# Kernel tuning notes

Measured on AMD Instinct MI355X. Metric: run time of the kernel, lower is better.

Reference implementation:

```python
import jax, jax.numpy as jnp
import numpy as np

IN_SIZE = 1024
HID = 2048
OUT = 1024
M_STEPS = 100   # max extra ponder steps -> up to M_STEPS+1 total steps
EPS = 0.01


def setup_inputs() -> dict:
    key = jax.random.key(0)
    ks = jax.random.split(key, 11)
    inv = 1.0 / np.sqrt(HID)

    def unif(k, shape, scale):
        return jax.random.uniform(k, shape, jnp.float32, -scale, scale)

    return {
        "x": jax.random.normal(ks[0], (IN_SIZE,), jnp.float32),
        "h0": jax.random.normal(ks[1], (HID,), jnp.float32) * 0.1,
        "c0": jax.random.normal(ks[2], (HID,), jnp.float32) * 0.1,
        "W_ih": unif(ks[3], (4 * HID, 1 + IN_SIZE), inv),
        "b_ih": unif(ks[4], (4 * HID,), inv),
        "W_hh": unif(ks[5], (4 * HID, HID), inv),
        "b_hh": unif(ks[6], (4 * HID,), inv),
        "w_halt": unif(ks[7], (HID,), inv),
        "b_halt": jnp.ones((1,), jnp.float32),  # fc_halt.bias = 1.0 per source
        "W_out": unif(ks[8], (OUT, HID), inv),
        "b_out": unif(ks[9], (OUT,), inv),
    }


def reference(x, h0, c0, W_ih, b_ih, W_hh, b_hh, w_halt, b_halt, W_out, b_out):
    # Input contribution is constant across steps except the prepended halt flag
    # (1 on first step, 0 after). Precompute it once.
    ih_x = W_ih[:, 1:] @ x + b_ih + b_hh      # (4H,)
    w_flag = W_ih[:, 0]                        # (4H,)

    def step(carry, flag):
        h, c = carry
        gates = ih_x + flag * w_flag + W_hh @ h  # (4H,)
        i, f, g, o = jnp.split(gates, 4)
        i = jax.nn.sigmoid(i)
        f = jax.nn.sigmoid(f)
        g = jnp.tanh(g)
        o = jax.nn.sigmoid(o)
        c = f * c + i * g
        h = o * jnp.tanh(c)
        return (h, c), (h, c)

    flags = jnp.concatenate(
        [jnp.ones((1,), x.dtype), jnp.zeros((M_STEPS,), x.dtype)])
    _, (H, C) = jax.lax.scan(step, (h0, c0), flags)  # (M+1, HID) each

    p = jax.nn.sigmoid(H @ w_halt + b_halt[0])       # (M+1,) halting probs
    csum = jnp.cumsum(p)
    halted = csum >= 1.0 - EPS
    # n = first step where cumulative halt prob crosses threshold, capped at M
    n = jnp.where(jnp.any(halted), jnp.argmax(halted), M_STEPS)
    # remainder r = 1 - sum(p[:n]); csum[n] - p[n] == sum(p[:n])
    r = 1.0 - jnp.where(n > 0, csum[n] - p[n], 0.0)

    idx = jnp.arange(M_STEPS + 1)
    w = jnp.where(idx < n, p, jnp.where(idx == n, r, 0.0))  # (M+1,)

    outputs = H @ W_out.T + b_out                    # (M+1, OUT)
    output = w @ outputs                             # (OUT,) weights sum to 1
    h_out = w @ H                                    # (HID,)
    c_out = w @ C                                    # (HID,)
    ponder = n.astype(x.dtype) + 1.0 + r
    return output, (h_out, c_out), ponder
```

## Files before the change

### kernel.cpp

```cpp
#include <hip/hip_runtime.h>


#define HID    2048
#define INS    1024
#define OUTS   1024
#define MSTEPS 100
#define NBLK   256
#define NTHR   1024
#define NWAVE  16
#define JPB    8
#define RPB    32

__device__ __forceinline__ float wave_reduce(float v) {
    #pragma unroll
    for (int off = 32; off > 0; off >>= 1)
        v += __shfl_down(v, off, 64);
    return v;
}


__global__ __launch_bounds__(NTHR) void alstm_kernel(
    const float* __restrict__ x,      const float* __restrict__ h0,
    const float* __restrict__ c0,     const float* __restrict__ W_ih,
    const float* __restrict__ b_ih,   const float* __restrict__ W_hh,
    const float* __restrict__ b_hh,   const float* __restrict__ w_halt,
    const float* __restrict__ b_halt, const float* __restrict__ W_out,
    const float* __restrict__ b_out,  float* __restrict__ out,
    float* __restrict__ ws)
{
    const int b    = blockIdx.x;
    const int tid  = threadIdx.x;
    const int wave = tid >> 6;
    const int lane = tid & 63;

    float*    slots  = ws;
    unsigned* bar    = (unsigned*)(ws + 128);
    float*    h_glob = ws + 256;
    float*    hbar_g = ws + 256 + HID;

    unsigned bar_target = 0;
    #define GBAR() do {                                                        \
        __syncthreads();                                                       \
        if (tid == 0) {                                                        \
            bar_target += NBLK;                                                \
            __hip_atomic_fetch_add(bar, 1u, __ATOMIC_ACQ_REL,                  \
                                   __HIP_MEMORY_SCOPE_AGENT);                  \
            while (__hip_atomic_load(bar, __ATOMIC_ACQUIRE,                    \
                                     __HIP_MEMORY_SCOPE_AGENT) < bar_target)   \
                __builtin_amdgcn_s_sleep(1);                                   \
        }                                                                      \
        __syncthreads();                                                       \
    } while (0)

    __shared__ float h_lds[HID];
    __shared__ float gate_lds[RPB];
    __shared__ float ihx_lds[RPB];
    __shared__ float wflag_lds[RPB];
    __shared__ float psum[NWAVE];

    const float bh = b_halt[0];
    const int j_own = b * JPB + tid;

    const int lr0 = 2 * wave;
    const int g   = lr0 >> 3;
    const int jj0 = lr0 & 7;
    const int r0  = g * HID + b * JPB + jj0;

    for (int k = tid; k < INS; k += NTHR) h_lds[k] = x[k];
    __syncthreads();

    #pragma unroll
    for (int rr = 0; rr < 2; ++rr) {
        const int r = r0 + rr;
        const float* wrow = W_ih + (size_t)r * (INS + 1) + 1;
        const int mis = (r + 1) & 3;
        const int p0  = (4 - mis) & 3;
        const int nv  = (INS - p0) >> 2;
        const float4* wv = (const float4*)(wrow + p0);
        float acc = 0.f;
        for (int i = lane; i < nv; i += 64) {
            float4 w4 = wv[i];
            int k = p0 + 4 * i;
            acc += w4.x * h_lds[k] + w4.y * h_lds[k + 1]
                 + w4.z * h_lds[k + 2] + w4.w * h_lds[k + 3];
        }
        if (lane == 0) {
            for (int k = 0; k < p0; ++k)            acc += wrow[k] * h_lds[k];
            for (int k = p0 + 4 * nv; k < INS; ++k) acc += wrow[k] * h_lds[k];
        }
        acc = wave_reduce(acc);
        if (lane == 0) {
            ihx_lds[lr0 + rr]   = acc + b_ih[r] + b_hh[r];
            wflag_lds[lr0 + rr] = W_ih[(size_t)r * (INS + 1)];
        }
    }

    float c_reg = 0.f, h_reg = 0.f, hbar = 0.f, cbar = 0.f;
    if (tid < JPB) c_reg = c0[j_own];

    float csum = 0.f, r_halt = 0.f;
    int   n_halt = 0;
    const float4* wrow0 = (const float4*)(W_hh + (size_t)r0 * HID);
    const float4* wrow1 = (const float4*)(W_hh + (size_t)(r0 + 1) * HID);

    for (int t = 0; t <= MSTEPS; ++t) {
        __syncthreads();
        const float* hsrc = (t == 0) ? h0 : h_glob;
        for (int k = tid; k < HID; k += NTHR) h_lds[k] = hsrc[k];
        __syncthreads();

        {
            const float4* hv = (const float4*)h_lds;
            float acc0 = 0.f, acc1 = 0.f;
            #pragma unroll
            for (int m = 0; m < HID / 256; ++m) {
                float4 hh = hv[lane + 64 * m];
                float4 w0 = wrow0[lane + 64 * m];
                float4 w1 = wrow1[lane + 64 * m];
                acc0 += w0.x * hh.x + w0.y * hh.y + w0.z * hh.z + w0.w * hh.w;
                acc1 += w1.x * hh.x + w1.y * hh.y + w1.z * hh.z + w1.w * hh.w;
            }
            acc0 = wave_reduce(acc0);
            acc1 = wave_reduce(acc1);
            if (lane == 0) {
                float b0 = ihx_lds[lr0], b1 = ihx_lds[lr0 + 1];
                if (t == 0) { b0 += wflag_lds[lr0]; b1 += wflag_lds[lr0 + 1]; }
                gate_lds[lr0]     = b0 + acc0;
                gate_lds[lr0 + 1] = b1 + acc1;
            }
        }
        __syncthreads();

        float part = 0.f;
        if (tid < JPB) {
            float iv = gate_lds[0 * JPB + tid];
            float fv = gate_lds[1 * JPB + tid];
            float gv = gate_lds[2 * JPB + tid];
            float ov = gate_lds[3 * JPB + tid];
            iv = 1.f / (1.f + expf(-iv));
            fv = 1.f / (1.f + expf(-fv));
            gv = tanhf(gv);
            ov = 1.f / (1.f + expf(-ov));
            c_reg = fv * c_reg + iv * gv;
            h_reg = ov * tanhf(c_reg);
            h_glob[j_own] = h_reg;
            part = h_reg * w_halt[j_own];
        }
        part += __shfl_down(part, 4, 64);
        part += __shfl_down(part, 2, 64);
        part += __shfl_down(part, 1, 64);
        if (tid == 0) atomicAdd(&slots[t], part);

        GBAR();

        float dotv = __hip_atomic_load(&slots[t], __ATOMIC_RELAXED,
                                       __HIP_MEMORY_SCOPE_AGENT);
        float p = 1.f / (1.f + expf(-(dotv + bh)));
        float prev = csum;
        csum += p;
        bool halt_now = (csum >= 1.f - 0.01f) || (t == MSTEPS);
        float wt = halt_now ? (1.f - prev) : p;
        if (tid < JPB) { hbar += wt * h_reg; cbar += wt * c_reg; }
        if (halt_now) { n_halt = t; r_halt = 1.f - prev; break; }
    }

    if (tid < JPB) {
        out[OUTS + j_own]       = hbar;
        out[OUTS + HID + j_own] = cbar;
        hbar_g[j_own] = hbar;
    }
    if (b == 0 && tid == 0) out[OUTS + 2 * HID] = (float)(n_halt + 1) + r_halt;

    GBAR();

    for (int k = tid; k < HID; k += NTHR) h_lds[k] = hbar_g[k];
    __syncthreads();

    {
        const int row = b * 4 + (wave & 3);
        const int q   = wave >> 2;
        const float4* wrow = (const float4*)(W_out + (size_t)row * HID) + q * 128;
        const float4* hv   = (const float4*)h_lds + q * 128;
        float acc = 0.f;
        #pragma unroll
        for (int m = 0; m < 2; ++m) {
            float4 wv4 = wrow[lane + 64 * m];
            float4 hh  = hv[lane + 64 * m];
            acc += wv4.x * hh.x + wv4.y * hh.y + wv4.z * hh.z + wv4.w * hh.w;
        }
        acc = wave_reduce(acc);
        if (lane == 0) psum[wave] = acc;
    }
    __syncthreads();
    if (tid < 4) {
        int row = b * 4 + tid;
        float s = psum[tid] + psum[tid + 4] + psum[tid + 8] + psum[tid + 12];
        out[row] = s + b_out[row];
    }
    #undef GBAR
}

extern "C" void kernel_launch(void* const* d_in, const int* in_sizes, int n_in,
                              void* d_out, int out_size, void* d_ws, size_t ws_size,
                              hipStream_t stream) {
    const float* x      = (const float*)d_in[0];
    const float* h0     = (const float*)d_in[1];
    const float* c0     = (const float*)d_in[2];
    const float* W_ih   = (const float*)d_in[3];
    const float* b_ih   = (const float*)d_in[4];
    const float* W_hh   = (const float*)d_in[5];
    const float* b_hh   = (const float*)d_in[6];
    const float* w_halt = (const float*)d_in[7];
    const float* b_halt = (const float*)d_in[8];
    const float* W_out  = (const float*)d_in[9];
    const float* b_out  = (const float*)d_in[10];
    float* out = (float*)d_out;
    float* ws  = (float*)d_ws;

    hipMemsetAsync(d_ws, 0, 1024, stream);

    alstm_kernel<<<dim3(NBLK), dim3(NTHR), 0, stream>>>(
        x, h0, c0, W_ih, b_ih, W_hh, b_hh, w_halt, b_halt, W_out, b_out,
        out, ws);
}
```

Baseline: 189.9 us.

## Keep W_hh and W_out rows in registers and double-buffer hidden state

Each wave now loads its two W_hh rows (64 floats per lane) and its W_out slice into registers once before the recurrence, so the ponder steps no longer re-read weights from global/L2. The global hidden-state buffer is double-buffered, which removes the extra __syncthreads at the top of each step. The h copy into LDS is collapsed to a single float2 per thread. The trade-off is higher register pressure at 1024 threads per block, which could cause spills.

```diff
diff --git a/kernel.cpp b/kernel.cpp
--- a/kernel.cpp
+++ b/kernel.cpp
@@ -35,8 +35,9 @@
 
     float*    slots  = ws;
     unsigned* bar    = (unsigned*)(ws + 128);
-    float*    h_glob = ws + 256;
-    float*    hbar_g = ws + 256 + HID;
+    float*    hbuf0  = ws + 256;
+    float*    hbuf1  = ws + 256 + HID;
+    float*    hbar_g = ws + 256 + 2 * HID;
 
     unsigned bar_target = 0;
     #define GBAR() do {                                                        \
@@ -65,6 +66,25 @@
     const int g   = lr0 >> 3;
     const int jj0 = lr0 & 7;
     const int r0  = g * HID + b * JPB + jj0;
+
+    float4 w0r[8], w1r[8];
+    {
+        const float4* wrow0 = (const float4*)(W_hh + (size_t)r0 * HID);
+        const float4* wrow1 = (const float4*)(W_hh + (size_t)(r0 + 1) * HID);
+        #pragma unroll
+        for (int m = 0; m < 8; ++m) {
+            w0r[m] = wrow0[lane + 64 * m];
+            w1r[m] = wrow1[lane + 64 * m];
+        }
+    }
+    const int orow = b * 4 + (wave & 3);
+    const int oq   = wave >> 2;
+    float4 wo0, wo1;
+    {
+        const float4* wor = (const float4*)(W_out + (size_t)orow * HID) + oq * 128;
+        wo0 = wor[lane];
+        wo1 = wor[lane + 64];
+    }
 
     for (int k = tid; k < INS; k += NTHR) h_lds[k] = x[k];
     __syncthreads();
@@ -97,28 +117,26 @@
 
     float c_reg = 0.f, h_reg = 0.f, hbar = 0.f, cbar = 0.f;
     if (tid < JPB) c_reg = c0[j_own];
+    __syncthreads();
 
     float csum = 0.f, r_halt = 0.f;
     int   n_halt = 0;
-    const float4* wrow0 = (const float4*)(W_hh + (size_t)r0 * HID);
-    const float4* wrow1 = (const float4*)(W_hh + (size_t)(r0 + 1) * HID);
-
     for (int t = 0; t <= MSTEPS; ++t) {
-        __syncthreads();
-        const float* hsrc = (t == 0) ? h0 : h_glob;
-        for (int k = tid; k < HID; k += NTHR) h_lds[k] = hsrc[k];
+        const float* hsrc = (t == 0) ? h0 : ((t & 1) ? hbuf1 : hbuf0);
+        float* hdst = ((t & 1) ? hbuf0 : hbuf1);
+        ((float2*)h_lds)[tid] = ((const float2*)hsrc)[tid];
         __syncthreads();
 
         {
             const float4* hv = (const float4*)h_lds;
             float acc0 = 0.f, acc1 = 0.f;
             #pragma unroll
-            for (int m = 0; m < HID / 256; ++m) {
+            for (int m = 0; m < 8; ++m) {
                 float4 hh = hv[lane + 64 * m];
-                float4 w0 = wrow0[lane + 64 * m];
-                float4 w1 = wrow1[lane + 64 * m];
-                acc0 += w0.x * hh.x + w0.y * hh.y + w0.z * hh.z + w0.w * hh.w;
-                acc1 += w1.x * hh.x + w1.y * hh.y + w1.z * hh.z + w1.w * hh.w;
+                acc0 += w0r[m].x * hh.x + w0r[m].y * hh.y
+                      + w0r[m].z * hh.z + w0r[m].w * hh.w;
+                acc1 += w1r[m].x * hh.x + w1r[m].y * hh.y
+                      + w1r[m].z * hh.z + w1r[m].w * hh.w;
             }
             acc0 = wave_reduce(acc0);
             acc1 = wave_reduce(acc1);
@@ -143,7 +161,7 @@
             ov = 1.f / (1.f + expf(-ov));
             c_reg = fv * c_reg + iv * gv;
             h_reg = ov * tanhf(c_reg);
-            h_glob[j_own] = h_reg;
+            hdst[j_own] = h_reg;
             part = h_reg * w_halt[j_own];
         }
         part += __shfl_down(part, 4, 64);
@@ -173,21 +191,14 @@
 
     GBAR();
 
-    for (int k = tid; k < HID; k += NTHR) h_lds[k] = hbar_g[k];
+    ((float2*)h_lds)[tid] = ((const float2*)hbar_g)[tid];
     __syncthreads();
 
     {
-        const int row = b * 4 + (wave & 3);
-        const int q   = wave >> 2;
-        const float4* wrow = (const float4*)(W_out + (size_t)row * HID) + q * 128;
-        const float4* hv   = (const float4*)h_lds + q * 128;
-        float acc = 0.f;
-        #pragma unroll
-        for (int m = 0; m < 2; ++m) {
-            float4 wv4 = wrow[lane + 64 * m];
-            float4 hh  = hv[lane + 64 * m];
-            acc += wv4.x * hh.x + wv4.y * hh.y + wv4.z * hh.z + wv4.w * hh.w;
-        }
+        const float4* hv = (const float4*)h_lds + oq * 128;
+        float4 h0v = hv[lane], h1v = hv[lane + 64];
+        float acc = wo0.x * h0v.x + wo0.y * h0v.y + wo0.z * h0v.z + wo0.w * h0v.w
+                  + wo1.x * h1v.x + wo1.y * h1v.y + wo1.z * h1v.z + wo1.w * h1v.w;
         acc = wave_reduce(acc);
         if (lane == 0) psum[wave] = acc;
     }
```

Measured after the change: 185.0 us. -2.5%, faster.

## Replace atomic grid barrier with tagged arrive/mailbox reduction through block 0

Applied to the files above, without the earlier changes.

Each block no longer does an atomic counter barrier plus a float atomicAdd. It now publishes its halting partial sum as a tagged 64-bit word. Block 0 gathers all 256 partials, reduces them and writes a tagged mailbox slot for each block, so the barrier and the halting-dot reduction become one round and float atomics go away. The hidden state is double-buffered so the next step's h load does not race with writers. The loop is also restructured so that h is loaded after the sync instead of at the top. In exchange, every step is serialized through block 0 with a gather-then-broadcast round trip, and correctness depends on the ordering between the fence and the relaxed stores.

```diff
diff --git a/kernel.cpp b/kernel.cpp
--- a/kernel.cpp
+++ b/kernel.cpp
@@ -11,11 +11,23 @@
 #define JPB    8
 #define RPB    32
 
+typedef unsigned long long u64;
+
 __device__ __forceinline__ float wave_reduce(float v) {
     #pragma unroll
     for (int off = 32; off > 0; off >>= 1)
         v += __shfl_down(v, off, 64);
     return v;
+}
+
+__device__ __forceinline__ u64 pack_tag(unsigned tag, float v) {
+    return ((u64)tag << 32) | (u64)__float_as_uint(v);
+}
+__device__ __forceinline__ u64 aload(const u64* p) {
+    return __hip_atomic_load(p, __ATOMIC_RELAXED, __HIP_MEMORY_SCOPE_AGENT);
+}
+__device__ __forceinline__ void astore(u64* p, u64 v) {
+    __hip_atomic_store(p, v, __ATOMIC_RELAXED, __HIP_MEMORY_SCOPE_AGENT);
 }
 
 
@@ -33,29 +45,19 @@
     const int wave = tid >> 6;
     const int lane = tid & 63;
 
-    float*    slots  = ws;
-    unsigned* bar    = (unsigned*)(ws + 128);
-    float*    h_glob = ws + 256;
-    float*    hbar_g = ws + 256 + HID;
-
-    unsigned bar_target = 0;
-    #define GBAR() do {                                                        \
-        __syncthreads();                                                       \
-        if (tid == 0) {                                                        \
-            bar_target += NBLK;                                                \
-            __hip_atomic_fetch_add(bar, 1u, __ATOMIC_ACQ_REL,                  \
-                                   __HIP_MEMORY_SCOPE_AGENT);                  \
-            while (__hip_atomic_load(bar, __ATOMIC_ACQUIRE,                    \
-                                     __HIP_MEMORY_SCOPE_AGENT) < bar_target)   \
-                __builtin_amdgcn_s_sleep(1);                                   \
-        }                                                                      \
-        __syncthreads();                                                       \
-    } while (0)
+    float* arrive = ws;
+    float* mail   = ws + 1024;
+    float* hbuf0  = ws + 2048;
+    float* hbuf1  = ws + 2048 + HID;
+    float* hbar_g = ws + 2048 + 2 * HID;
 
     __shared__ float h_lds[HID];
+    __shared__ float x_lds[INS];
     __shared__ float gate_lds[RPB];
     __shared__ float ihx_lds[RPB];
     __shared__ float wflag_lds[RPB];
+    __shared__ float red_lds[4];
+    __shared__ float bcast_lds;
     __shared__ float psum[NWAVE];
 
     const float bh = b_halt[0];
@@ -66,7 +68,41 @@
     const int jj0 = lr0 & 7;
     const int r0  = g * HID + b * JPB + jj0;
 
-    for (int k = tid; k < INS; k += NTHR) h_lds[k] = x[k];
+    #define SYNC_ROUND(tag_, part_, dot_) do {                                 \
+        if (tid == 0) {                                                        \
+            __threadfence();        \
+            astore((u64*)(arrive + 4 * b), pack_tag((tag_), (part_)));         \
+        }                                                                      \
+        if (b == 0) {                                                          \
+            float pf = 0.f;                                                    \
+            if (tid < NBLK) {                                                  \
+                u64 v;                                                         \
+                do { v = aload((u64*)(arrive + 4 * tid)); }                    \
+                while ((unsigned)(v >> 32) != (tag_));                         \
+                pf = __uint_as_float((unsigned)v);                             \
+            }                                                                  \
+            float s = wave_reduce(pf);                                         \
+            if (lane == 0 && wave < 4) red_lds[wave] = s;                      \
+            __syncthreads();                                                   \
+            if (tid == 0)                                                      \
+                bcast_lds = red_lds[0] + red_lds[1] + red_lds[2] + red_lds[3]; \
+            __syncthreads();                                                   \
+            if (tid < NBLK)                                                    \
+                astore((u64*)(mail + 4 * tid), pack_tag((tag_), bcast_lds));   \
+        }                                                                      \
+        if (tid == 0) {                                                        \
+            u64 v;                                                             \
+            do { v = aload((u64*)(mail + 4 * b)); }                            \
+            while ((unsigned)(v >> 32) != (tag_));                             \
+            bcast_lds = __uint_as_float((unsigned)v);                          \
+            __threadfence();        \
+        }                                                                      \
+        __syncthreads();                                                       \
+        (dot_) = bcast_lds;                                                    \
+    } while (0)
+
+    if (tid < INS / 2) ((float2*)x_lds)[tid] = ((const float2*)x)[tid];
+    ((float2*)h_lds)[tid] = ((const float2*)h0)[tid];
     __syncthreads();
 
     #pragma unroll
@@ -81,12 +117,12 @@
         for (int i = lane; i < nv; i += 64) {
             float4 w4 = wv[i];
             int k = p0 + 4 * i;
-            acc += w4.x * h_lds[k] + w4.y * h_lds[k + 1]
-                 + w4.z * h_lds[k + 2] + w4.w * h_lds[k + 3];
+            acc += w4.x * x_lds[k] + w4.y * x_lds[k + 1]
+                 + w4.z * x_lds[k + 2] + w4.w * x_lds[k + 3];
         }
         if (lane == 0) {
-            for (int k = 0; k < p0; ++k)            acc += wrow[k] * h_lds[k];
-            for (int k = p0 + 4 * nv; k < INS; ++k) acc += wrow[k] * h_lds[k];
+            for (int k = 0; k < p0; ++k)            acc += wrow[k] * x_lds[k];
+            for (int k = p0 + 4 * nv; k < INS; ++k) acc += wrow[k] * x_lds[k];
         }
         acc = wave_reduce(acc);
         if (lane == 0) {
@@ -98,22 +134,17 @@
     float c_reg = 0.f, h_reg = 0.f, hbar = 0.f, cbar = 0.f;
     if (tid < JPB) c_reg = c0[j_own];
 
+    const float4* wrow0 = (const float4*)(W_hh + (size_t)r0 * HID);
+    const float4* wrow1 = (const float4*)(W_hh + (size_t)(r0 + 1) * HID);
+
     float csum = 0.f, r_halt = 0.f;
     int   n_halt = 0;
-    const float4* wrow0 = (const float4*)(W_hh + (size_t)r0 * HID);
-    const float4* wrow1 = (const float4*)(W_hh + (size_t)(r0 + 1) * HID);
-
     for (int t = 0; t <= MSTEPS; ++t) {
-        __syncthreads();
-        const float* hsrc = (t == 0) ? h0 : h_glob;
-        for (int k = tid; k < HID; k += NTHR) h_lds[k] = hsrc[k];
-        __syncthreads();
-
         {
             const float4* hv = (const float4*)h_lds;
             float acc0 = 0.f, acc1 = 0.f;
             #pragma unroll
-            for (int m = 0; m < HID / 256; ++m) {
+            for (int m = 0; m < 8; ++m) {
                 float4 hh = hv[lane + 64 * m];
                 float4 w0 = wrow0[lane + 64 * m];
                 float4 w1 = wrow1[lane + 64 * m];
@@ -132,6 +163,7 @@
         __syncthreads();
 
         float part = 0.f;
+        float* hdst = (t & 1) ? hbuf1 : hbuf0;
         if (tid < JPB) {
             float iv = gate_lds[0 * JPB + tid];
             float fv = gate_lds[1 * JPB + tid];
@@ -143,18 +175,16 @@
             ov = 1.f / (1.f + expf(-ov));
             c_reg = fv * c_reg + iv * gv;
             h_reg = ov * tanhf(c_reg);
-            h_glob[j_own] = h_reg;
+            hdst[j_own] = h_reg;
             part = h_reg * w_halt[j_own];
         }
         part += __shfl_down(part, 4, 64);
         part += __shfl_down(part, 2, 64);
         part += __shfl_down(part, 1, 64);
-        if (tid == 0) atomicAdd(&slots[t], part);
-
-        GBAR();
-
-        float dotv = __hip_atomic_load(&slots[t], __ATOMIC_RELAXED,
-                                       __HIP_MEMORY_SCOPE_AGENT);
+
+        float dotv;
+        SYNC_ROUND(t + 1, part, dotv);
+
         float p = 1.f / (1.f + expf(-(dotv + bh)));
         float prev = csum;
         csum += p;
@@ -162,6 +192,10 @@
         float wt = halt_now ? (1.f - prev) : p;
         if (tid < JPB) { hbar += wt * h_reg; cbar += wt * c_reg; }
         if (halt_now) { n_halt = t; r_halt = 1.f - prev; break; }
+
+        __syncthreads();
+        ((float2*)h_lds)[tid] = ((const float2*)hdst)[tid];
+        __syncthreads();
     }
 
     if (tid < JPB) {
@@ -171,9 +205,12 @@
     }
     if (b == 0 && tid == 0) out[OUTS + 2 * HID] = (float)(n_halt + 1) + r_halt;
 
-    GBAR();
-
-    for (int k = tid; k < HID; k += NTHR) h_lds[k] = hbar_g[k];
+    float dummy;
+    SYNC_ROUND(n_halt + 2, 0.f, dummy);
+    (void)dummy;
+
+    __syncthreads();
+    ((float2*)h_lds)[tid] = ((const float2*)hbar_g)[tid];
     __syncthreads();
 
     {
@@ -181,13 +218,10 @@
         const int q   = wave >> 2;
         const float4* wrow = (const float4*)(W_out + (size_t)row * HID) + q * 128;
         const float4* hv   = (const float4*)h_lds + q * 128;
-        float acc = 0.f;
-        #pragma unroll
-        for (int m = 0; m < 2; ++m) {
-            float4 wv4 = wrow[lane + 64 * m];
-            float4 hh  = hv[lane + 64 * m];
-            acc += wv4.x * hh.x + wv4.y * hh.y + wv4.z * hh.z + wv4.w * hh.w;
-        }
+        float4 w0 = wrow[lane],      h0v = hv[lane];
+        float4 w1 = wrow[lane + 64], h1v = hv[lane + 64];
+        float acc = w0.x * h0v.x + w0.y * h0v.y + w0.z * h0v.z + w0.w * h0v.w
+                  + w1.x * h1v.x + w1.y * h1v.y + w1.z * h1v.z + w1.w * h1v.w;
         acc = wave_reduce(acc);
         if (lane == 0) psum[wave] = acc;
     }
@@ -197,7 +231,7 @@
         float s = psum[tid] + psum[tid + 4] + psum[tid + 8] + psum[tid + 12];
         out[row] = s + b_out[row];
     }
-    #undef GBAR
+    #undef SYNC_ROUND
 }
 
 extern "C" void kernel_launch(void* const* d_in, const int* in_sizes, int n_in,
@@ -217,7 +251,7 @@
     float* out = (float*)d_out;
     float* ws  = (float*)d_ws;
 
-    hipMemsetAsync(d_ws, 0, 1024, stream);
+    hipMemsetAsync(d_ws, 0, 8192, stream);
 
     alstm_kernel<<<dim3(NBLK), dim3(NTHR), 0, stream>>>(
         x, h0, c0, W_ih, b_ih, W_hh, b_hh, w_halt, b_halt, W_out, b_out,
```

Result: faster. 178.5 us (-6.0%).
